# Optimization experiments

Measured on AMD Instinct MI355X. Metric: run time of the kernel, lower is better.

Reference implementation:

```python
import jax, jax.numpy as jnp
import numpy as np

IN_DIM = 1024
HID = 1024


def setup_inputs() -> dict:
    key = jax.random.key(0)
    ks = jax.random.split(key, 20)
    u = lambda k, shape: jax.random.uniform(k, shape, jnp.float32, -0.1, 0.1)
    inp = {
        "x": jax.random.normal(ks[0], (32, 512, IN_DIM), jnp.float32),
        "h0": jnp.zeros((1, 32, HID), jnp.float32),
        "c0": jnp.zeros((1, 32, HID), jnp.float32),
        "W_ii": u(ks[1], (IN_DIM, HID)), "W_if": u(ks[2], (IN_DIM, HID)),
        "W_ig": u(ks[3], (IN_DIM, HID)), "W_io": u(ks[4], (IN_DIM, HID)),
        "W_hi": u(ks[5], (HID, HID)), "W_hf": u(ks[6], (HID, HID)),
        "W_hg": u(ks[7], (HID, HID)), "W_ho": u(ks[8], (HID, HID)),
        "b_ii": u(ks[9], (HID,)), "b_if": u(ks[10], (HID,)),
        "b_ig": u(ks[11], (HID,)), "b_io": u(ks[12], (HID,)),
        "b_hi": u(ks[13], (HID,)), "b_hf": u(ks[14], (HID,)),
        "b_hg": u(ks[15], (HID,)), "b_ho": u(ks[16], (HID,)),
    }
    return inp


def _lstm(x, h0, c0, W_ii, W_if, W_ig, W_io, W_hi, W_hf, W_hg, W_ho,
          b_ii, b_if, b_ig, b_io, b_hi, b_hf, b_hg, b_ho):
    # Precompute all input projections in one big GEMM per gate: [B,S,H]
    xi = jnp.einsum('bsd,dh->bsh', x, W_ii) + b_ii + b_hi
    xf = jnp.einsum('bsd,dh->bsh', x, W_if) + b_if + b_hf
    xg = jnp.einsum('bsd,dh->bsh', x, W_ig) + b_ig + b_hg
    xo = jnp.einsum('bsd,dh->bsh', x, W_io) + b_io + b_ho
    # stack over time for scan: [S, B, H]
    xs = (jnp.swapaxes(xi, 0, 1), jnp.swapaxes(xf, 0, 1),
          jnp.swapaxes(xg, 0, 1), jnp.swapaxes(xo, 0, 1))

    def step(carry, xt):
        h, c = carry
        xti, xtf, xtg, xto = xt
        i = jax.nn.sigmoid(xti + h @ W_hi)
        f = jax.nn.sigmoid(xtf + h @ W_hf)
        g = jnp.tanh(xtg + h @ W_hg)
        o = jax.nn.sigmoid(xto + h @ W_ho)
        c = f * c + i * g
        h = o * jnp.tanh(c)
        return (h, c), h

    (ht, ct), ys = jax.lax.scan(step, (h0[0], c0[0]), xs)
    output = jnp.swapaxes(ys, 0, 1)  # [B, S, H]
    return output, (ht, ct)


def reference(x, h0, c0, W_ii, W_if, W_ig, W_io, W_hi, W_hf, W_hg, W_ho,
              b_ii, b_if, b_ig, b_io, b_hi, b_hf, b_hg, b_ho):
    return _lstm(x, h0, c0, W_ii, W_if, W_ig, W_io, W_hi, W_hf, W_hg, W_ho,
                 b_ii, b_if, b_ig, b_io, b_hi, b_hf, b_hg, b_ho)
```

## Files before the change

kernel.cpp:

```cpp
#include <hip/hip_runtime.h>
#include <cstdint>
#include <cstddef>

typedef __attribute__((ext_vector_type(8))) short s16x8;
typedef __attribute__((ext_vector_type(4))) float f32x4;

#define HID 1024
#define BATCH 32
#define SEQ 512

__device__ __forceinline__ short f2bf(float f){
  unsigned u = __builtin_bit_cast(unsigned, f);
  u = (u + 0x7fffu + ((u >> 16) & 1u)) >> 16;
  return (short)u;
}
__device__ __forceinline__ float bf2f(short s){
  unsigned u = ((unsigned)(unsigned short)s) << 16;
  return __builtin_bit_cast(float, u);
}

__global__ __launch_bounds__(256) void pack_x_kernel(const float* __restrict__ x,
                                                     s16x8* __restrict__ xpk){
  int P = blockIdx.x * 256 + threadIdx.x;
  int lane = P & 63;
  int w = (P >> 6) & 15; int ks = w >> 3, mt = w & 7;
  int tile = P >> 10; int kt = tile & 15; int mb = tile >> 4;
  int row = mb * 128 + mt * 16 + (lane & 15);
  int k0 = kt * 64 + ks * 32 + (lane >> 4) * 8;
  const f32x4* src = (const f32x4*)(x + (size_t)row * HID + k0);
  f32x4 v0 = src[0], v1 = src[1];
  s16x8 o;
  o[0]=f2bf(v0[0]); o[1]=f2bf(v0[1]); o[2]=f2bf(v0[2]); o[3]=f2bf(v0[3]);
  o[4]=f2bf(v1[0]); o[5]=f2bf(v1[1]); o[6]=f2bf(v1[2]); o[7]=f2bf(v1[3]);
  xpk[P] = o;
}

__global__ __launch_bounds__(256) void pack_wx_kernel(const float* __restrict__ Wii,
    const float* __restrict__ Wif, const float* __restrict__ Wig,
    const float* __restrict__ Wio, s16x8* __restrict__ wxpk){
  int P = blockIdx.x * 256 + threadIdx.x;
  int lane = P & 63;
  int w = (P >> 6) & 15; int ks = w >> 3, nt = w & 7;
  int tile = P >> 10; int kt = tile & 15; int nb = tile >> 4;
  int n = nb * 128 + nt * 16 + (lane & 15);
  int g = n >> 10, c = n & 1023;
  int k0 = kt * 64 + ks * 32 + (lane >> 4) * 8;
  const float* W = (g == 0) ? Wii : (g == 1) ? Wif : (g == 2) ? Wig : Wio;
  s16x8 o;
  #pragma unroll
  for (int j = 0; j < 8; ++j) o[j] = f2bf(W[(size_t)(k0 + j) * HID + c]);
  wxpk[P] = o;
}

__global__ __launch_bounds__(256) void pack_wh_kernel(const float* __restrict__ Whi,
    const float* __restrict__ Whf, const float* __restrict__ Whg,
    const float* __restrict__ Who, s16x8* __restrict__ whpk){
  int P = blockIdx.x * 256 + threadIdx.x;
  int lane = P & 63;
  int q = P >> 6;
  int nt = q & 1; int ks = (q >> 1) & 1; int kt = (q >> 2) & 15; int wg = q >> 6;
  int col16 = lane & 15;
  int g = nt * 2 + (col16 >> 3);
  int c = wg * 8 + (col16 & 7);
  int k0 = kt * 64 + ks * 32 + (lane >> 4) * 8;
  const float* W = (g == 0) ? Whi : (g == 1) ? Whf : (g == 2) ? Whg : Who;
  s16x8 o;
  #pragma unroll
  for (int j = 0; j < 8; ++j) o[j] = f2bf(W[(size_t)(k0 + j) * HID + c]);
  whpk[P] = o;
}

__global__ __launch_bounds__(256) void init_kernel(const float* __restrict__ h0,
    const float* __restrict__ c0,
    const float* bii, const float* bif, const float* big, const float* bio,
    const float* bhi, const float* bhf, const float* bhg, const float* bho,
    float* __restrict__ bias_sum, s16x8* __restrict__ hA0, float* __restrict__ c_state){
  int T = blockIdx.x * 256 + threadIdx.x;
  if (T < 4096){
    int g = T >> 10, c = T & 1023;
    const float* bi = (g == 0) ? bii : (g == 1) ? bif : (g == 2) ? big : bio;
    const float* bh = (g == 0) ? bhi : (g == 1) ? bhf : (g == 2) ? bhg : bho;
    bias_sum[T] = bi[c] + bh[c];
  } else if (T < 8192){
    int u = T - 4096;
    int lane = u & 63; int q = u >> 6;
    int kstep = q & 31; int mtb = q >> 5;
    int b = mtb * 16 + (lane & 15);
    int col0 = kstep * 32 + (lane >> 4) * 8;
    const float* src = h0 + (size_t)b * HID + col0;
    s16x8 o;
    #pragma unroll
    for (int j = 0; j < 8; ++j) o[j] = f2bf(src[j]);
    hA0[u] = o;
  } else if (T < 12288){
    int u = T - 8192;
    const f32x4* s = (const f32x4*)(c0 + (size_t)u * 8);
    f32x4* d = (f32x4*)(c_state + (size_t)u * 8);
    d[0] = s[0]; d[1] = s[1];
  }
}

__global__ __launch_bounds__(256) void gemm_xp_kernel(const s16x8* __restrict__ xpk,
    const s16x8* __restrict__ wxpk, const float* __restrict__ bias_sum,
    short* __restrict__ XP){
  const int mb = blockIdx.x, nb = blockIdx.y;
  const int tid = threadIdx.x, lane = tid & 63, wave = tid >> 6;
  const int wr = wave >> 1, wc = wave & 1;
  __shared__ s16x8 sA[1024];
  __shared__ s16x8 sB[1024];
  f32x4 acc[4][4] = {};
  const s16x8* gA = xpk + (size_t)(mb * 16) * 1024;
  const s16x8* gB = wxpk + (size_t)(nb * 16) * 1024;
  for (int kt = 0; kt < 16; ++kt){
    __syncthreads();
    #pragma unroll
    for (int i = 0; i < 4; ++i){
      sA[i * 256 + tid] = gA[(size_t)kt * 1024 + i * 256 + tid];
      sB[i * 256 + tid] = gB[(size_t)kt * 1024 + i * 256 + tid];
    }
    __syncthreads();
    #pragma unroll
    for (int ks = 0; ks < 2; ++ks){
      s16x8 af[4], bfr[4];
      #pragma unroll
      for (int i = 0; i < 4; ++i) af[i] = sA[(ks * 8 + wr * 4 + i) * 64 + lane];
      #pragma unroll
      for (int j = 0; j < 4; ++j) bfr[j] = sB[(ks * 8 + wc * 4 + j) * 64 + lane];
      #pragma unroll
      for (int i = 0; i < 4; ++i)
        #pragma unroll
        for (int j = 0; j < 4; ++j)
          acc[i][j] = __builtin_amdgcn_mfma_f32_16x16x32_bf16(af[i], bfr[j], acc[i][j], 0, 0, 0);
    }
  }
  #pragma unroll
  for (int i = 0; i < 4; ++i){
    const int m_base = mb * 128 + (wr * 4 + i) * 16 + ((lane >> 4) << 2);
    #pragma unroll
    for (int j = 0; j < 4; ++j){
      const int n = nb * 128 + (wc * 4 + j) * 16 + (lane & 15);
      const float bias = bias_sum[n];
      const int g = n >> 10, c = n & 1023;
      #pragma unroll
      for (int r = 0; r < 4; ++r){
        const int m = m_base + r;
        const int tt = m & 511, bb = m >> 9;
        XP[(((size_t)((tt * 32 + bb) * 4 + g)) << 10) + c] = f2bf(acc[i][j][r] + bias);
      }
    }
  }
}

__global__ __launch_bounds__(256) void lstm_step_kernel(const s16x8* __restrict__ whpk,
    const s16x8* __restrict__ hprev, s16x8* __restrict__ hnext,
    const short* __restrict__ XP, float* __restrict__ c_state,
    float* __restrict__ out, float* __restrict__ htct, int t)
{
  const int wg = blockIdx.x;
  const int tid = threadIdx.x, lane = tid & 63, wave = tid >> 6;
  const int mt = wave >> 1, nt = wave & 1;
  __shared__ float pre[32][32];
  f32x4 acc = {0.f, 0.f, 0.f, 0.f};
  const s16x8* B = whpk + (size_t)wg * 4096;
  #pragma unroll
  for (int kk = 0; kk < 32; ++kk){
    s16x8 a = hprev[(mt * 32 + kk) * 64 + lane];
    s16x8 b = B[(kk * 2 + nt) * 64 + lane];
    acc = __builtin_amdgcn_mfma_f32_16x16x32_bf16(a, b, acc, 0, 0, 0);
  }
  const int col16 = lane & 15;
  const int prow = mt * 16 + ((lane >> 4) << 2);
  const int pcol = nt * 16 + col16;
  pre[prow + 0][pcol] = acc[0];
  pre[prow + 1][pcol] = acc[1];
  pre[prow + 2][pcol] = acc[2];
  pre[prow + 3][pcol] = acc[3];
  __syncthreads();
  const int b = tid >> 3, cc = tid & 7;
  const int hcol = wg * 8 + cc;
  const size_t xpbase = ((size_t)t * 32 + b) * 4096;
  float p0 = pre[b][0 * 8 + cc] + bf2f(XP[xpbase + 0 * 1024 + hcol]);
  float p1 = pre[b][1 * 8 + cc] + bf2f(XP[xpbase + 1 * 1024 + hcol]);
  float p2 = pre[b][2 * 8 + cc] + bf2f(XP[xpbase + 2 * 1024 + hcol]);
  float p3 = pre[b][3 * 8 + cc] + bf2f(XP[xpbase + 3 * 1024 + hcol]);
  float ig = 1.f / (1.f + __expf(-p0));
  float fg = 1.f / (1.f + __expf(-p1));
  float gg = tanhf(p2);
  float og = 1.f / (1.f + __expf(-p3));
  float cp = c_state[b * HID + hcol];
  float cn = fg * cp + ig * gg;
  float h  = og * tanhf(cn);
  c_state[b * HID + hcol] = cn;
  out[((size_t)b * SEQ + t) * HID + hcol] = h;
  int kstep = hcol >> 5, hi = (hcol >> 3) & 3, j = hcol & 7, l16 = b & 15, bmt = b >> 4;
  ((short*)hnext)[(((bmt * 32 + kstep) * 64 + hi * 16 + l16) << 3) + j] = f2bf(h);
  if (t == SEQ - 1){
    htct[b * HID + hcol] = h;
    htct[32 * HID + b * HID + hcol] = cn;
  }
}

extern "C" void kernel_launch(void* const* d_in, const int* in_sizes, int n_in,
                              void* d_out, int out_size, void* d_ws, size_t ws_size,
                              hipStream_t stream){
  const float* x   = (const float*)d_in[0];
  const float* h0  = (const float*)d_in[1];
  const float* c0  = (const float*)d_in[2];
  const float* Wii = (const float*)d_in[3];
  const float* Wif = (const float*)d_in[4];
  const float* Wig = (const float*)d_in[5];
  const float* Wio = (const float*)d_in[6];
  const float* Whi = (const float*)d_in[7];
  const float* Whf = (const float*)d_in[8];
  const float* Whg = (const float*)d_in[9];
  const float* Who = (const float*)d_in[10];
  const float* bii = (const float*)d_in[11];
  const float* bif = (const float*)d_in[12];
  const float* big = (const float*)d_in[13];
  const float* bio = (const float*)d_in[14];
  const float* bhi = (const float*)d_in[15];
  const float* bhf = (const float*)d_in[16];
  const float* bhg = (const float*)d_in[17];
  const float* bho = (const float*)d_in[18];

  char* ws = (char*)d_ws;
  s16x8* xpk      = (s16x8*)(ws);
  s16x8* wxpk     = (s16x8*)(ws + 33554432ull);
  s16x8* whpk     = (s16x8*)(ws + 41943040ull);
  short* XP       = (short*)(ws + 50331648ull);
  s16x8* hA0      = (s16x8*)(ws + 184549376ull);
  s16x8* hA1      = (s16x8*)(ws + 184614912ull);
  float* c_state  = (float*)(ws + 184680448ull);
  float* bias_sum = (float*)(ws + 184811520ull);

  float* out  = (float*)d_out;
  float* htct = out + (size_t)BATCH * SEQ * HID;

  pack_x_kernel<<<8192, 256, 0, stream>>>(x, xpk);
  pack_wx_kernel<<<2048, 256, 0, stream>>>(Wii, Wif, Wig, Wio, wxpk);
  pack_wh_kernel<<<2048, 256, 0, stream>>>(Whi, Whf, Whg, Who, whpk);
  init_kernel<<<48, 256, 0, stream>>>(h0, c0, bii, bif, big, bio,
                                      bhi, bhf, bhg, bho, bias_sum, hA0, c_state);
  gemm_xp_kernel<<<dim3(128, 32), 256, 0, stream>>>(xpk, wxpk, bias_sum, XP);
  for (int t = 0; t < SEQ; ++t){
    const s16x8* hp = (t & 1) ? hA1 : hA0;
    s16x8*       hn = (t & 1) ? hA0 : hA1;
    lstm_step_kernel<<<128, 256, 0, stream>>>(whpk, hp, hn, XP, c_state, out, htct, t);
  }
}
```

Before: 3.011 ms.

## Replace per-step launches with a persistent cooperative LSTM kernel

The 512 separate per-timestep launches become a single cooperative kernel. Each block keeps its recurrent weight slice in LDS, holds the cell state in registers, and steps through time with a grid.sync between steps. The XP layout is switched to gate-interleaved so each thread reads its four gate preactivations in one 8-byte load. This removes launch overhead and repeated global weight reads, but each step now pays for a grid-wide barrier and relies on all 128 blocks being co-resident.

```diff
diff --git a/kernel.cpp b/kernel.cpp
--- a/kernel.cpp
+++ b/kernel.cpp
@@ -1,8 +1,12 @@
 #include <hip/hip_runtime.h>
+#include <hip/hip_cooperative_groups.h>
 #include <cstdint>
 #include <cstddef>
 
+namespace cg = cooperative_groups;
+
 typedef __attribute__((ext_vector_type(8))) short s16x8;
+typedef __attribute__((ext_vector_type(4))) short s16x4;
 typedef __attribute__((ext_vector_type(4))) float f32x4;
 
 #define HID 1024
@@ -71,10 +75,9 @@
 }
 
 __global__ __launch_bounds__(256) void init_kernel(const float* __restrict__ h0,
-    const float* __restrict__ c0,
     const float* bii, const float* bif, const float* big, const float* bio,
     const float* bhi, const float* bhf, const float* bhg, const float* bho,
-    float* __restrict__ bias_sum, s16x8* __restrict__ hA0, float* __restrict__ c_state){
+    float* __restrict__ bias_sum, s16x8* __restrict__ hA0){
   int T = blockIdx.x * 256 + threadIdx.x;
   if (T < 4096){
     int g = T >> 10, c = T & 1023;
@@ -92,11 +95,6 @@
     #pragma unroll
     for (int j = 0; j < 8; ++j) o[j] = f2bf(src[j]);
     hA0[u] = o;
-  } else if (T < 12288){
-    int u = T - 8192;
-    const f32x4* s = (const f32x4*)(c0 + (size_t)u * 8);
-    f32x4* d = (f32x4*)(c_state + (size_t)u * 8);
-    d[0] = s[0]; d[1] = s[1];
   }
 }
 
@@ -145,58 +143,78 @@
       for (int r = 0; r < 4; ++r){
         const int m = m_base + r;
         const int tt = m & 511, bb = m >> 9;
-        XP[(((size_t)((tt * 32 + bb) * 4 + g)) << 10) + c] = f2bf(acc[i][j][r] + bias);
+        XP[(((size_t)(tt * 32 + bb) << 10) + c) * 4 + g] = f2bf(acc[i][j][r] + bias);
       }
     }
   }
 }
 
-__global__ __launch_bounds__(256) void lstm_step_kernel(const s16x8* __restrict__ whpk,
-    const s16x8* __restrict__ hprev, s16x8* __restrict__ hnext,
-    const short* __restrict__ XP, float* __restrict__ c_state,
-    float* __restrict__ out, float* __restrict__ htct, int t)
+__global__ __launch_bounds__(256, 1) void lstm_rec_kernel(const s16x8* __restrict__ whpk,
+    s16x8* __restrict__ hA, s16x8* __restrict__ hB, const short* __restrict__ XP,
+    const float* __restrict__ c0, float* __restrict__ out, float* __restrict__ htct)
 {
+  extern __shared__ char smem[];
+  s16x8* sW  = (s16x8*)smem;
+  float* pre = (float*)(smem + 65536);
+  cg::grid_group grid = cg::this_grid();
+
   const int wg = blockIdx.x;
   const int tid = threadIdx.x, lane = tid & 63, wave = tid >> 6;
   const int mt = wave >> 1, nt = wave & 1;
-  __shared__ float pre[32][32];
-  f32x4 acc = {0.f, 0.f, 0.f, 0.f};
-  const s16x8* B = whpk + (size_t)wg * 4096;
-  #pragma unroll
-  for (int kk = 0; kk < 32; ++kk){
-    s16x8 a = hprev[(mt * 32 + kk) * 64 + lane];
-    s16x8 b = B[(kk * 2 + nt) * 64 + lane];
-    acc = __builtin_amdgcn_mfma_f32_16x16x32_bf16(a, b, acc, 0, 0, 0);
-  }
-  const int col16 = lane & 15;
-  const int prow = mt * 16 + ((lane >> 4) << 2);
-  const int pcol = nt * 16 + col16;
-  pre[prow + 0][pcol] = acc[0];
-  pre[prow + 1][pcol] = acc[1];
-  pre[prow + 2][pcol] = acc[2];
-  pre[prow + 3][pcol] = acc[3];
-  __syncthreads();
+
+  {
+    const s16x8* gW = whpk + (size_t)wg * 4096;
+    #pragma unroll
+    for (int i = 0; i < 16; ++i) sW[i * 256 + tid] = gW[i * 256 + tid];
+  }
+
   const int b = tid >> 3, cc = tid & 7;
   const int hcol = wg * 8 + cc;
-  const size_t xpbase = ((size_t)t * 32 + b) * 4096;
-  float p0 = pre[b][0 * 8 + cc] + bf2f(XP[xpbase + 0 * 1024 + hcol]);
-  float p1 = pre[b][1 * 8 + cc] + bf2f(XP[xpbase + 1 * 1024 + hcol]);
-  float p2 = pre[b][2 * 8 + cc] + bf2f(XP[xpbase + 2 * 1024 + hcol]);
-  float p3 = pre[b][3 * 8 + cc] + bf2f(XP[xpbase + 3 * 1024 + hcol]);
-  float ig = 1.f / (1.f + __expf(-p0));
-  float fg = 1.f / (1.f + __expf(-p1));
-  float gg = tanhf(p2);
-  float og = 1.f / (1.f + __expf(-p3));
-  float cp = c_state[b * HID + hcol];
-  float cn = fg * cp + ig * gg;
-  float h  = og * tanhf(cn);
-  c_state[b * HID + hcol] = cn;
-  out[((size_t)b * SEQ + t) * HID + hcol] = h;
-  int kstep = hcol >> 5, hi = (hcol >> 3) & 3, j = hcol & 7, l16 = b & 15, bmt = b >> 4;
-  ((short*)hnext)[(((bmt * 32 + kstep) * 64 + hi * 16 + l16) << 3) + j] = f2bf(h);
-  if (t == SEQ - 1){
-    htct[b * HID + hcol] = h;
-    htct[32 * HID + b * HID + hcol] = cn;
+  float c = c0[b * HID + hcol];
+  const int kstep = hcol >> 5, hi = (hcol >> 3) & 3, jj = hcol & 7;
+  const size_t hoff = (((size_t)((b >> 4) * 32 + kstep) * 64 + hi * 16 + (b & 15)) << 3) + jj;
+
+  const int prow = mt * 16 + ((lane >> 4) << 2);
+  const int pcol = nt * 16 + (lane & 15);
+
+  const s16x8* h_cur = hA;
+  s16x8* h_nxt = hB;
+
+  __syncthreads();
+
+  for (int t = 0; t < SEQ; ++t){
+    f32x4 acc = {0.f, 0.f, 0.f, 0.f};
+    #pragma unroll
+    for (int kk = 0; kk < 32; ++kk){
+      s16x8 a = h_cur[(mt * 32 + kk) * 64 + lane];
+      s16x8 w = sW[(kk * 2 + nt) * 64 + lane];
+      acc = __builtin_amdgcn_mfma_f32_16x16x32_bf16(a, w, acc, 0, 0, 0);
+    }
+    pre[(prow + 0) * 33 + pcol] = acc[0];
+    pre[(prow + 1) * 33 + pcol] = acc[1];
+    pre[(prow + 2) * 33 + pcol] = acc[2];
+    pre[(prow + 3) * 33 + pcol] = acc[3];
+    __syncthreads();
+
+    s16x4 xp = *(const s16x4*)(XP + ((((size_t)t * 32 + b) << 10) + hcol) * 4);
+    float p0 = pre[b * 33 + 0 * 8 + cc] + bf2f(xp[0]);
+    float p1 = pre[b * 33 + 1 * 8 + cc] + bf2f(xp[1]);
+    float p2 = pre[b * 33 + 2 * 8 + cc] + bf2f(xp[2]);
+    float p3 = pre[b * 33 + 3 * 8 + cc] + bf2f(xp[3]);
+    float ig = 1.f / (1.f + __expf(-p0));
+    float fg = 1.f / (1.f + __expf(-p1));
+    float gg = tanhf(p2);
+    float og = 1.f / (1.f + __expf(-p3));
+    c = fg * c + ig * gg;
+    float h = og * tanhf(c);
+    out[((size_t)b * SEQ + t) * HID + hcol] = h;
+    ((short*)h_nxt)[hoff] = f2bf(h);
+    if (t == SEQ - 1){
+      htct[b * HID + hcol] = h;
+      htct[32 * HID + b * HID + hcol] = c;
+    }
+    s16x8* tmp = (s16x8*)h_cur; h_cur = h_nxt; h_nxt = tmp;
+    grid.sync();
   }
 }
 
@@ -230,7 +248,6 @@
   short* XP       = (short*)(ws + 50331648ull);
   s16x8* hA0      = (s16x8*)(ws + 184549376ull);
   s16x8* hA1      = (s16x8*)(ws + 184614912ull);
-  float* c_state  = (float*)(ws + 184680448ull);
   float* bias_sum = (float*)(ws + 184811520ull);
 
   float* out  = (float*)d_out;
@@ -239,12 +256,12 @@
   pack_x_kernel<<<8192, 256, 0, stream>>>(x, xpk);
   pack_wx_kernel<<<2048, 256, 0, stream>>>(Wii, Wif, Wig, Wio, wxpk);
   pack_wh_kernel<<<2048, 256, 0, stream>>>(Whi, Whf, Whg, Who, whpk);
-  init_kernel<<<48, 256, 0, stream>>>(h0, c0, bii, bif, big, bio,
-                                      bhi, bhf, bhg, bho, bias_sum, hA0, c_state);
+  init_kernel<<<32, 256, 0, stream>>>(h0, bii, bif, big, bio,
+                                      bhi, bhf, bhg, bho, bias_sum, hA0);
   gemm_xp_kernel<<<dim3(128, 32), 256, 0, stream>>>(xpk, wxpk, bias_sum, XP);
-  for (int t = 0; t < SEQ; ++t){
-    const s16x8* hp = (t & 1) ? hA1 : hA0;
-    s16x8*       hn = (t & 1) ? hA0 : hA1;
-    lstm_step_kernel<<<128, 256, 0, stream>>>(whpk, hp, hn, XP, c_state, out, htct, t);
-  }
-}
+
+  void* args[] = {(void*)&whpk, (void*)&hA0, (void*)&hA1, (void*)&XP,
+                  (void*)&c0, (void*)&out, (void*)&htct};
+  hipLaunchCooperativeKernel((const void*)lstm_rec_kernel, dim3(128), dim3(256),
+                             args, 65536 + 32 * 33 * 4, stream);
+}
```

After: 9.295 ms. 3.09x slower.
